# Kernel tuning notes

Measured on AMD Instinct MI355X. Metric: run time of the kernel, lower is better.

Reference implementation:

```python
import jax, jax.numpy as jnp
import numpy as np

# Config: 4 sparse batch items, each with 2048 active voxels (uniform-length case
# of sparse full self-attention). channels=1024, heads=16, head_dim=64.
B_SEQ, L, H, D = 4, 2048, 16, 64
C = H * D  # 1024
N = B_SEQ * L  # 8192
EPS = 1e-12  # F.normalize eps


def setup_inputs() -> dict:
    key = jax.random.key(0)
    ks = jax.random.split(key, 6)
    s = 1.0 / np.sqrt(C)
    return {
        "x": jax.random.normal(ks[0], (N, C), dtype=jnp.float32),
        "W_qkv": jax.random.normal(ks[1], (C, 3 * C), dtype=jnp.float32) * s,
        "b_qkv": jnp.zeros((3 * C,), dtype=jnp.float32),
        "gamma_q": jnp.ones((H, D), dtype=jnp.float32),
        "gamma_k": jnp.ones((H, D), dtype=jnp.float32),
        "W_out": jax.random.normal(ks[2], (C, C), dtype=jnp.float32) * s,
        "b_out": jnp.zeros((C,), dtype=jnp.float32),
    }


def _qk_rms_norm(t, gamma):
    # SparseMultiHeadRMSNorm: L2-normalize last dim, scale by gamma[h,d] * sqrt(D)
    norm = jnp.maximum(jnp.linalg.norm(t, axis=-1, keepdims=True), EPS)
    return (t / norm) * gamma * (D ** 0.5)


def reference(x, W_qkv, b_qkv, gamma_q, gamma_k, W_out, b_out):
    qkv = x @ W_qkv + b_qkv                       # [N, 3C]
    qkv = qkv.reshape(B_SEQ, L, 3, H, D)          # fused pre-reshape
    q, k, v = qkv[:, :, 0], qkv[:, :, 1], qkv[:, :, 2]  # [B,L,H,D]
    q = _qk_rms_norm(q, gamma_q)
    k = _qk_rms_norm(k, gamma_k)
    # full scaled dot-product attention within each sparse batch item
    scores = jnp.einsum('blhd,bmhd->bhlm', q, k) / (D ** 0.5)
    attn = jax.nn.softmax(scores, axis=-1)
    h = jnp.einsum('bhlm,bmhd->blhd', attn, v)    # [B,L,H,D]
    h = h.reshape(N, C)
    return h @ W_out + b_out
```

## Files before the change

### kernel.cpp

```cpp
#include <hip/hip_runtime.h>

using u16 = unsigned short;

typedef float  f32x4  __attribute__((ext_vector_type(4)));
typedef float  f32x16 __attribute__((ext_vector_type(16)));
typedef __bf16 bf16x8 __attribute__((ext_vector_type(8)));
typedef short  s16x8  __attribute__((ext_vector_type(8)));

#define DEVI __device__ __forceinline__

constexpr int TOK = 8192;
constexpr int CIN = 1024;
constexpr int C3  = 3072;
constexpr int NH  = 16;
constexpr int HD  = 64;
constexpr int SL  = 2048;
constexpr int BH  = 64;

constexpr float LOG2E = 1.4426950408889634f;

DEVI u16 f2bf(float x) {
  unsigned u = __builtin_bit_cast(unsigned, x);
  u += 0x7FFFu + ((u >> 16) & 1u);
  return (u16)(u >> 16);
}

DEVI f32x4 mfma16(s16x8 a, s16x8 b, f32x4 c) {
  return __builtin_amdgcn_mfma_f32_16x16x32_bf16(
      __builtin_bit_cast(bf16x8, a), __builtin_bit_cast(bf16x8, b), c, 0, 0, 0);
}

DEVI f32x16 mfma32(s16x8 a, s16x8 b, f32x16 c) {
  return __builtin_amdgcn_mfma_f32_32x32x16_bf16(
      __builtin_bit_cast(bf16x8, a), __builtin_bit_cast(bf16x8, b), c, 0, 0, 0);
}

DEVI void gload_lds16(const void* g, void* l) {
  __builtin_amdgcn_global_load_lds(
      (const __attribute__((address_space(1))) unsigned int*)g,
      (__attribute__((address_space(3))) unsigned int*)l, 16, 0, 0);
}

DEVI unsigned cvtpk(float lo, float hi) {
  unsigned r;
  asm("v_cvt_pk_bf16_f32 %0, %1, %2" : "=v"(r) : "v"(lo), "v"(hi));
  return r;
}

DEVI void plswap(unsigned& a, unsigned& b) {
  asm("v_permlane32_swap_b32 %0, %1" : "+v"(a), "+v"(b));
}

__global__ __launch_bounds__(256) void k_cvt_x(const float* __restrict__ x,
                                               u16* __restrict__ xb) {
  const int total = TOK * CIN / 4;
  for (int i = blockIdx.x * 256 + threadIdx.x; i < total; i += gridDim.x * 256) {
    float4 v = ((const float4*)x)[i];
    ushort4 o;
    o.x = f2bf(v.x); o.y = f2bf(v.y); o.z = f2bf(v.z); o.w = f2bf(v.w);
    ((ushort4*)xb)[i] = o;
  }
}

__global__ __launch_bounds__(256) void k_transpose(const float* __restrict__ in,
                                                   u16* __restrict__ out,
                                                   int R, int C) {
  __shared__ u16 t[64][72];
  int rt = R >> 6;
  int tr = (blockIdx.x % rt) << 6;
  int tc = (blockIdx.x / rt) << 6;
  int tid = threadIdx.x;
#pragma unroll
  for (int k2 = 0; k2 < 16; k2++) {
    int idx = k2 * 256 + tid;
    int r = idx >> 6, c = idx & 63;
    t[r][c] = f2bf(in[(size_t)(tr + r) * C + tc + c]);
  }
  __syncthreads();
#pragma unroll
  for (int k2 = 0; k2 < 16; k2++) {
    int idx = k2 * 256 + tid;
    int r = idx >> 6, c = idx & 63;
    out[(size_t)(tc + r) * R + tr + c] = t[c][r];
  }
}

__global__ __launch_bounds__(256) void k_gemm_qkv(
    const u16* __restrict__ A, const u16* __restrict__ Bt,
    const float* __restrict__ bias, const float* __restrict__ gq,
    const float* __restrict__ gk,
    u16* __restrict__ Qn, u16* __restrict__ Kn, u16* __restrict__ Vt) {
  constexpr int BK = 32, K = 1024, NT = C3 / 128;
  __shared__ u16 As[128 * BK], Bs[128 * BK];
  const int bm = (blockIdx.x / NT) * 128, bn = (blockIdx.x % NT) * 128;
  const int tid = threadIdx.x, lane = tid & 63, w = tid >> 6;
  const int l15 = lane & 15, g = lane >> 4;
  const int wr = (w >> 1) * 64, wc = (w & 1) * 64;

  f32x4 acc[4][4];
#pragma unroll
  for (int i = 0; i < 4; i++)
#pragma unroll
    for (int j = 0; j < 4; j++) acc[i][j] = f32x4{0.f, 0.f, 0.f, 0.f};

  const int srow = tid >> 2, scol = (tid & 3) * 8;
  const u16* Ag = A + (size_t)(bm + srow) * K + scol;
  const u16* Bg = Bt + (size_t)(bn + srow) * K + scol;
  char* AsB = (char*)As;
  char* BsB = (char*)Bs;

  for (int k0 = 0; k0 < K; k0 += BK) {
    __syncthreads();
    gload_lds16(Ag + k0,          AsB + w * 1024);
    gload_lds16(Ag + 64 * K + k0, AsB + 4096 + w * 1024);
    gload_lds16(Bg + k0,          BsB + w * 1024);
    gload_lds16(Bg + 64 * K + k0, BsB + 4096 + w * 1024);
    __syncthreads();
    s16x8 af[4], bf[4];
#pragma unroll
    for (int mf = 0; mf < 4; mf++)
      af[mf] = *(const s16x8*)(As + (wr + mf * 16 + l15) * BK + g * 8);
#pragma unroll
    for (int nf = 0; nf < 4; nf++)
      bf[nf] = *(const s16x8*)(Bs + (wc + nf * 16 + l15) * BK + g * 8);
#pragma unroll
    for (int mf = 0; mf < 4; mf++)
#pragma unroll
      for (int nf = 0; nf < 4; nf++)
        acc[mf][nf] = mfma16(af[mf], bf[nf], acc[mf][nf]);
  }

  const int c0 = bn + wc;
  const int sec = c0 >> 10;
  const int head = (c0 & 1023) >> 6;
  float bv[4], gv[4];
#pragma unroll
  for (int nf = 0; nf < 4; nf++) {
    bv[nf] = bias[c0 + nf * 16 + l15];
    gv[nf] = 1.f;
    if (sec == 0) gv[nf] = gq[head * 64 + nf * 16 + l15];
    if (sec == 1) gv[nf] = gk[head * 64 + nf * 16 + l15];
  }
#pragma unroll
  for (int mf = 0; mf < 4; mf++) {
#pragma unroll
    for (int nf = 0; nf < 4; nf++)
#pragma unroll
      for (int r = 0; r < 4; r++) acc[mf][nf][r] += bv[nf];
    if (sec < 2) {
#pragma unroll
      for (int r = 0; r < 4; r++) {
        float ss = 0.f;
#pragma unroll
        for (int nf = 0; nf < 4; nf++) ss += acc[mf][nf][r] * acc[mf][nf][r];
        ss += __shfl_xor(ss, 1); ss += __shfl_xor(ss, 2);
        ss += __shfl_xor(ss, 4); ss += __shfl_xor(ss, 8);
        float nrm = fmaxf(sqrtf(ss), 1e-12f);
        float f = (sec == 0 ? LOG2E : 8.0f) / nrm;
#pragma unroll
        for (int nf = 0; nf < 4; nf++) acc[mf][nf][r] *= f;
      }
    }
    int rbase = bm + wr + mf * 16 + 4 * g;
#pragma unroll
    for (int r = 0; r < 4; r++) {
      int row = rbase + r;
      int b = row >> 11, tok = row & 2047;
      int bh = b * NH + head;
#pragma unroll
      for (int nf = 0; nf < 4; nf++) {
        int d = nf * 16 + l15;
        u16 val = f2bf(acc[mf][nf][r] * gv[nf]);
        if (sec == 0)      Qn[((size_t)bh * SL + tok) * HD + d] = val;
        else if (sec == 1) Kn[((size_t)bh * SL + tok) * HD + d] = val;
        else               Vt[((size_t)bh * HD + d) * SL + tok] = val;
      }
    }
  }
}

__global__ __launch_bounds__(512) void k_attn(const u16* __restrict__ Qn,
                                              const u16* __restrict__ Kn,
                                              const u16* __restrict__ Vt,
                                              u16* __restrict__ hm) {
  __shared__ __align__(16) char KL[2][8192];
  __shared__ __align__(16) char VL[2][8192];
  const int bh = blockIdx.x & 63, qb = blockIdx.x >> 6;
  const int tid = threadIdx.x, w = tid >> 6, lane = tid & 63;
  const int l31 = lane & 31, h = lane >> 5;
  const int qr0 = qb * 256 + w * 32;

  const int sr  = tid >> 3;
  const int scb = ((tid & 7) << 4) ^ ((sr & 7) << 4);
  const char* kst = (const char*)(Kn + (size_t)bh * SL * HD) + (size_t)sr * 128 + scb;
  const char* vst = (const char*)(Vt + (size_t)bh * HD * SL) + (size_t)sr * 4096 + scb;
  char* kl0 = KL[0] + (w << 10);
  char* vl0 = VL[0] + (w << 10);
  char* kl1 = KL[1] + (w << 10);
  char* vl1 = VL[1] + (w << 10);

  const u16* Qb = Qn + ((size_t)bh * SL + qr0 + l31) * HD + 8 * h;
  s16x8 qf[4];
#pragma unroll
  for (int ks = 0; ks < 4; ks++) qf[ks] = *(const s16x8*)(Qb + ks * 16);

  const int lb = l31 * 128 + ((h << 4) ^ ((l31 & 7) << 4));

  f32x16 o0, o1;
#pragma unroll
  for (int i = 0; i < 16; i++) { o0[i] = 0.f; o1[i] = 0.f; }
  float mr = -1e30f, lr = 0.f;

  gload_lds16(kst, kl0);
  gload_lds16(vst, vl0);
  __syncthreads();

  for (int it = 0; it < 32; ++it) {
    const char* KB = (it & 1) ? KL[1] : KL[0];
    const char* VB = (it & 1) ? VL[1] : VL[0];
    if (it < 31) {
      const size_t ko = (size_t)(it + 1) << 13;
      const size_t vo = (size_t)(it + 1) << 7;
      gload_lds16(kst + ko, (it & 1) ? kl0 : kl1);
      gload_lds16(vst + vo, (it & 1) ? vl0 : vl1);
    }

    f32x16 s0, s1;
#pragma unroll
    for (int i = 0; i < 16; i++) { s0[i] = 0.f; s1[i] = 0.f; }
    __builtin_amdgcn_s_setprio(1);
#pragma unroll
    for (int ks = 0; ks < 4; ks++) {
      const s16x8 ka  = *(const s16x8*)(KB + (lb ^ (ks << 5)));
      const s16x8 kb2 = *(const s16x8*)(KB + 4096 + (lb ^ (ks << 5)));
      s0 = mfma32(ka, qf[ks], s0);
      s1 = mfma32(kb2, qf[ks], s1);
    }
    __builtin_amdgcn_s_setprio(0);

    float mx8[8];
#pragma unroll
    for (int i = 0; i < 8; i++)
      mx8[i] = fmaxf(fmaxf(s0[i], s0[i + 8]), fmaxf(s1[i], s1[i + 8]));
    float m0 = fmaxf(fmaxf(mx8[0], mx8[1]), fmaxf(mx8[2], mx8[3]));
    float m1 = fmaxf(fmaxf(mx8[4], mx8[5]), fmaxf(mx8[6], mx8[7]));
    float bm = fmaxf(m0, m1);
    bm = fmaxf(bm, __shfl_xor(bm, 32));

    if (!__all(bm <= mr + 8.f)) {
      const float mn = fmaxf(mr, bm);
      const float sc = __builtin_amdgcn_exp2f(mr - mn);
      mr = mn;
      lr *= sc;
#pragma unroll
      for (int i = 0; i < 16; i++) { o0[i] *= sc; o1[i] *= sc; }
    }
#pragma unroll
    for (int i = 0; i < 16; i++) s0[i] = __builtin_amdgcn_exp2f(s0[i] - mr);
#pragma unroll
    for (int i = 0; i < 16; i++) s1[i] = __builtin_amdgcn_exp2f(s1[i] - mr);
    float sm8[8];
#pragma unroll
    for (int i = 0; i < 8; i++)
      sm8[i] = (s0[i] + s0[i + 8]) + (s1[i] + s1[i + 8]);
    lr += ((sm8[0] + sm8[1]) + (sm8[2] + sm8[3])) +
          ((sm8[4] + sm8[5]) + (sm8[6] + sm8[7]));

    union PBu { unsigned u[4]; s16x8 v; } pb;
#define MK_PB(SV, B)                              \
    {                                             \
      unsigned a0 = cvtpk(SV[B + 0], SV[B + 1]);  \
      unsigned c0 = cvtpk(SV[B + 4], SV[B + 5]);  \
      plswap(a0, c0);                             \
      unsigned a1 = cvtpk(SV[B + 2], SV[B + 3]);  \
      unsigned c1 = cvtpk(SV[B + 6], SV[B + 7]);  \
      plswap(a1, c1);                             \
      pb.u[0] = a0; pb.u[1] = a1; pb.u[2] = c0; pb.u[3] = c1; \
    }
#define PV_STEP(KS)                                            \
    {                                                          \
      const s16x8 va = *(const s16x8*)(VB + (lb ^ (KS << 5))); \
      const s16x8 vb = *(const s16x8*)(VB + 4096 + (lb ^ (KS << 5))); \
      __builtin_amdgcn_s_setprio(1);                           \
      o0 = mfma32(va, pb.v, o0);                               \
      o1 = mfma32(vb, pb.v, o1);                               \
      __builtin_amdgcn_s_setprio(0);                           \
    }
    MK_PB(s0, 0) PV_STEP(0)
    MK_PB(s0, 8) PV_STEP(1)
    MK_PB(s1, 0) PV_STEP(2)
    MK_PB(s1, 8) PV_STEP(3)
#undef MK_PB
#undef PV_STEP

    __syncthreads();
  }

  const float ltot = lr + __shfl_xor(lr, 32);
  const float inv = 1.f / ltot;
  const int bq = bh >> 4, hh = bh & 15;
  u16* hb = hm + ((size_t)bq * SL + qr0 + l31) * CIN + hh * HD;
#pragma unroll
  for (int rg = 0; rg < 4; rg++) {
    const int d0 = 8 * rg + 4 * h;
    unsigned lo = cvtpk(o0[4 * rg + 0] * inv, o0[4 * rg + 1] * inv);
    unsigned hi = cvtpk(o0[4 * rg + 2] * inv, o0[4 * rg + 3] * inv);
    *(unsigned long long*)(hb + d0) =
        (unsigned long long)lo | ((unsigned long long)hi << 32);
    unsigned lo1 = cvtpk(o1[4 * rg + 0] * inv, o1[4 * rg + 1] * inv);
    unsigned hi1 = cvtpk(o1[4 * rg + 2] * inv, o1[4 * rg + 3] * inv);
    *(unsigned long long*)(hb + 32 + d0) =
        (unsigned long long)lo1 | ((unsigned long long)hi1 << 32);
  }
}

__global__ __launch_bounds__(256) void k_gemm_out(
    const u16* __restrict__ A, const u16* __restrict__ Bt,
    const float* __restrict__ bias, float* __restrict__ out) {
  constexpr int BK = 32, K = 1024, NT = CIN / 128;
  __shared__ u16 As[128 * BK], Bs[128 * BK];
  const int bm = (blockIdx.x / NT) * 128, bn = (blockIdx.x % NT) * 128;
  const int tid = threadIdx.x, lane = tid & 63, w = tid >> 6;
  const int l15 = lane & 15, g = lane >> 4;
  const int wr = (w >> 1) * 64, wc = (w & 1) * 64;

  f32x4 acc[4][4];
#pragma unroll
  for (int i = 0; i < 4; i++)
#pragma unroll
    for (int j = 0; j < 4; j++) acc[i][j] = f32x4{0.f, 0.f, 0.f, 0.f};

  const int srow = tid >> 2, scol = (tid & 3) * 8;
  const u16* Ag = A + (size_t)(bm + srow) * K + scol;
  const u16* Bg = Bt + (size_t)(bn + srow) * K + scol;
  char* AsB = (char*)As;
  char* BsB = (char*)Bs;

  for (int k0 = 0; k0 < K; k0 += BK) {
    __syncthreads();
    gload_lds16(Ag + k0,          AsB + w * 1024);
    gload_lds16(Ag + 64 * K + k0, AsB + 4096 + w * 1024);
    gload_lds16(Bg + k0,          BsB + w * 1024);
    gload_lds16(Bg + 64 * K + k0, BsB + 4096 + w * 1024);
    __syncthreads();
    s16x8 af[4], bf[4];
#pragma unroll
    for (int mf = 0; mf < 4; mf++)
      af[mf] = *(const s16x8*)(As + (wr + mf * 16 + l15) * BK + g * 8);
#pragma unroll
    for (int nf = 0; nf < 4; nf++)
      bf[nf] = *(const s16x8*)(Bs + (wc + nf * 16 + l15) * BK + g * 8);
#pragma unroll
    for (int mf = 0; mf < 4; mf++)
#pragma unroll
      for (int nf = 0; nf < 4; nf++)
        acc[mf][nf] = mfma16(af[mf], bf[nf], acc[mf][nf]);
  }

  float bv[4];
#pragma unroll
  for (int nf = 0; nf < 4; nf++) bv[nf] = bias[bn + wc + nf * 16 + l15];
#pragma unroll
  for (int mf = 0; mf < 4; mf++)
#pragma unroll
    for (int r = 0; r < 4; r++) {
      int row = bm + wr + mf * 16 + 4 * g + r;
#pragma unroll
      for (int nf = 0; nf < 4; nf++)
        out[(size_t)row * CIN + bn + wc + nf * 16 + l15] = acc[mf][nf][r] + bv[nf];
    }
}

extern "C" void kernel_launch(void* const* d_in, const int* in_sizes, int n_in,
                              void* d_out, int out_size, void* d_ws, size_t ws_size,
                              hipStream_t stream) {
  const float* x    = (const float*)d_in[0];
  const float* Wqkv = (const float*)d_in[1];
  const float* bqkv = (const float*)d_in[2];
  const float* gq   = (const float*)d_in[3];
  const float* gk   = (const float*)d_in[4];
  const float* Wout = (const float*)d_in[5];
  const float* bout = (const float*)d_in[6];
  float* out = (float*)d_out;

  char* ws = (char*)d_ws;
  u16* xb  = (u16*)(ws);
  u16* wqT = (u16*)(ws + 16777216);
  u16* woT = (u16*)(ws + 23068672);
  u16* Qn  = (u16*)(ws + 25165824);
  u16* Kn  = (u16*)(ws + 41943040);
  u16* Vt  = (u16*)(ws + 58720256);
  u16* hm  = (u16*)(ws + 75497472);

  k_cvt_x<<<2048, 256, 0, stream>>>(x, xb);
  k_transpose<<<(1024 / 64) * (3072 / 64), 256, 0, stream>>>(Wqkv, wqT, 1024, 3072);
  k_transpose<<<(1024 / 64) * (1024 / 64), 256, 0, stream>>>(Wout, woT, 1024, 1024);
  k_gemm_qkv<<<(TOK / 128) * (C3 / 128), 256, 0, stream>>>(xb, wqT, bqkv, gq, gk, Qn, Kn, Vt);
  k_attn<<<BH * (SL / 256), 512, 0, stream>>>(Qn, Kn, Vt, hm);
  k_gemm_out<<<(TOK / 128) * (CIN / 128), 256, 0, stream>>>(hm, woT, bout, out);
}
```

Baseline: 228.5 us.

## Double-buffer LDS tiles in QKV and output GEMMs to overlap loads with MFMA

Both projection GEMMs now keep two LDS buffers and issue the global-to-LDS loads for the next K-slice before the MFMAs on the current slice. This removes one barrier per iteration and hides global load latency behind compute. The MFMA block is also wrapped in s_setprio to raise wave priority during matrix math. LDS use per block doubles, which may reduce occupancy. Correctness depends on the async LDS loads completing before the single barrier at the end of each iteration.

```diff
diff --git a/kernel.cpp b/kernel.cpp
--- a/kernel.cpp
+++ b/kernel.cpp
@@ -90,8 +90,8 @@
     const float* __restrict__ bias, const float* __restrict__ gq,
     const float* __restrict__ gk,
     u16* __restrict__ Qn, u16* __restrict__ Kn, u16* __restrict__ Vt) {
-  constexpr int BK = 32, K = 1024, NT = C3 / 128;
-  __shared__ u16 As[128 * BK], Bs[128 * BK];
+  constexpr int BK = 32, K = 1024, NT = C3 / 128, NIT = K / BK;
+  __shared__ u16 As[2][128 * BK], Bs[2][128 * BK];
   const int bm = (blockIdx.x / NT) * 128, bn = (blockIdx.x % NT) * 128;
   const int tid = threadIdx.x, lane = tid & 63, w = tid >> 6;
   const int l15 = lane & 15, g = lane >> 4;
@@ -106,29 +106,40 @@
   const int srow = tid >> 2, scol = (tid & 3) * 8;
   const u16* Ag = A + (size_t)(bm + srow) * K + scol;
   const u16* Bg = Bt + (size_t)(bn + srow) * K + scol;
-  char* AsB = (char*)As;
-  char* BsB = (char*)Bs;
-
-  for (int k0 = 0; k0 < K; k0 += BK) {
+
+#define STAGE_G1(BUF, K0)                                            \
+  {                                                                  \
+    char* AsB = (char*)As[BUF];                                      \
+    char* BsB = (char*)Bs[BUF];                                      \
+    gload_lds16(Ag + (K0),          AsB + w * 1024);                 \
+    gload_lds16(Ag + 64 * K + (K0), AsB + 4096 + w * 1024);          \
+    gload_lds16(Bg + (K0),          BsB + w * 1024);                 \
+    gload_lds16(Bg + 64 * K + (K0), BsB + 4096 + w * 1024);          \
+  }
+
+  STAGE_G1(0, 0)
+  __syncthreads();
+
+  for (int t = 0; t < NIT; ++t) {
+    const int cur = t & 1;
+    if (t < NIT - 1) STAGE_G1(cur ^ 1, (t + 1) * BK)
+    s16x8 af[4], bfx[4];
+#pragma unroll
+    for (int mf = 0; mf < 4; mf++)
+      af[mf] = *(const s16x8*)(As[cur] + (wr + mf * 16 + l15) * BK + g * 8);
+#pragma unroll
+    for (int nf = 0; nf < 4; nf++)
+      bfx[nf] = *(const s16x8*)(Bs[cur] + (wc + nf * 16 + l15) * BK + g * 8);
+    __builtin_amdgcn_s_setprio(1);
+#pragma unroll
+    for (int mf = 0; mf < 4; mf++)
+#pragma unroll
+      for (int nf = 0; nf < 4; nf++)
+        acc[mf][nf] = mfma16(af[mf], bfx[nf], acc[mf][nf]);
+    __builtin_amdgcn_s_setprio(0);
     __syncthreads();
-    gload_lds16(Ag + k0,          AsB + w * 1024);
-    gload_lds16(Ag + 64 * K + k0, AsB + 4096 + w * 1024);
-    gload_lds16(Bg + k0,          BsB + w * 1024);
-    gload_lds16(Bg + 64 * K + k0, BsB + 4096 + w * 1024);
-    __syncthreads();
-    s16x8 af[4], bf[4];
-#pragma unroll
-    for (int mf = 0; mf < 4; mf++)
-      af[mf] = *(const s16x8*)(As + (wr + mf * 16 + l15) * BK + g * 8);
-#pragma unroll
-    for (int nf = 0; nf < 4; nf++)
-      bf[nf] = *(const s16x8*)(Bs + (wc + nf * 16 + l15) * BK + g * 8);
-#pragma unroll
-    for (int mf = 0; mf < 4; mf++)
-#pragma unroll
-      for (int nf = 0; nf < 4; nf++)
-        acc[mf][nf] = mfma16(af[mf], bf[nf], acc[mf][nf]);
-  }
+  }
+#undef STAGE_G1
 
   const int c0 = bn + wc;
   const int sec = c0 >> 10;
@@ -317,8 +328,8 @@
 __global__ __launch_bounds__(256) void k_gemm_out(
     const u16* __restrict__ A, const u16* __restrict__ Bt,
     const float* __restrict__ bias, float* __restrict__ out) {
-  constexpr int BK = 32, K = 1024, NT = CIN / 128;
-  __shared__ u16 As[128 * BK], Bs[128 * BK];
+  constexpr int BK = 32, K = 1024, NT = CIN / 128, NIT = K / BK;
+  __shared__ u16 As[2][128 * BK], Bs[2][128 * BK];
   const int bm = (blockIdx.x / NT) * 128, bn = (blockIdx.x % NT) * 128;
   const int tid = threadIdx.x, lane = tid & 63, w = tid >> 6;
   const int l15 = lane & 15, g = lane >> 4;
@@ -333,29 +344,40 @@
   const int srow = tid >> 2, scol = (tid & 3) * 8;
   const u16* Ag = A + (size_t)(bm + srow) * K + scol;
   const u16* Bg = Bt + (size_t)(bn + srow) * K + scol;
-  char* AsB = (char*)As;
-  char* BsB = (char*)Bs;
-
-  for (int k0 = 0; k0 < K; k0 += BK) {
+
+#define STAGE_G2(BUF, K0)                                            \
+  {                                                                  \
+    char* AsB = (char*)As[BUF];                                      \
+    char* BsB = (char*)Bs[BUF];                                      \
+    gload_lds16(Ag + (K0),          AsB + w * 1024);                 \
+    gload_lds16(Ag + 64 * K + (K0), AsB + 4096 + w * 1024);          \
+    gload_lds16(Bg + (K0),          BsB + w * 1024);                 \
+    gload_lds16(Bg + 64 * K + (K0), BsB + 4096 + w * 1024);          \
+  }
+
+  STAGE_G2(0, 0)
+  __syncthreads();
+
+  for (int t = 0; t < NIT; ++t) {
+    const int cur = t & 1;
+    if (t < NIT - 1) STAGE_G2(cur ^ 1, (t + 1) * BK)
+    s16x8 af[4], bfx[4];
+#pragma unroll
+    for (int mf = 0; mf < 4; mf++)
+      af[mf] = *(const s16x8*)(As[cur] + (wr + mf * 16 + l15) * BK + g * 8);
+#pragma unroll
+    for (int nf = 0; nf < 4; nf++)
+      bfx[nf] = *(const s16x8*)(Bs[cur] + (wc + nf * 16 + l15) * BK + g * 8);
+    __builtin_amdgcn_s_setprio(1);
+#pragma unroll
+    for (int mf = 0; mf < 4; mf++)
+#pragma unroll
+      for (int nf = 0; nf < 4; nf++)
+        acc[mf][nf] = mfma16(af[mf], bfx[nf], acc[mf][nf]);
+    __builtin_amdgcn_s_setprio(0);
     __syncthreads();
-    gload_lds16(Ag + k0,          AsB + w * 1024);
-    gload_lds16(Ag + 64 * K + k0, AsB + 4096 + w * 1024);
-    gload_lds16(Bg + k0,          BsB + w * 1024);
-    gload_lds16(Bg + 64 * K + k0, BsB + 4096 + w * 1024);
-    __syncthreads();
-    s16x8 af[4], bf[4];
-#pragma unroll
-    for (int mf = 0; mf < 4; mf++)
-      af[mf] = *(const s16x8*)(As + (wr + mf * 16 + l15) * BK + g * 8);
-#pragma unroll
-    for (int nf = 0; nf < 4; nf++)
-      bf[nf] = *(const s16x8*)(Bs + (wc + nf * 16 + l15) * BK + g * 8);
-#pragma unroll
-    for (int mf = 0; mf < 4; mf++)
-#pragma unroll
-      for (int nf = 0; nf < 4; nf++)
-        acc[mf][nf] = mfma16(af[mf], bf[nf], acc[mf][nf]);
-  }
+  }
+#undef STAGE_G2
 
   float bv[4];
 #pragma unroll
```

After: 244.2 us. 1.07x slower.

## Rewrite QKV and output GEMMs with 256x128 tiles and triple-buffered LDS pipeline

Applied to the files above, without the earlier changes.

Both projection GEMMs now use 512-thread blocks with 256x128 output tiles and a K step of 64. Global-to-LDS copies are triple-buffered with explicit vmcnt waits so loads overlap MFMA work, and the LDS layout is XOR-swizzled to avoid bank conflicts. Block indices are remapped so neighbouring blocks share input tiles in L2, and wave priority is raised around the MFMA bursts. In exchange, each block uses about 147KB of LDS, which limits occupancy to a single block per CU.

```diff
diff --git a/kernel.cpp b/kernel.cpp
--- a/kernel.cpp
+++ b/kernel.cpp
@@ -85,17 +85,77 @@
   }
 }
 
-__global__ __launch_bounds__(256) void k_gemm_qkv(
+#define STAGE6(BUF, KT)                                                  \
+  { char* Ld = L + (BUF) * 49152;                                        \
+    const size_t ko = (size_t)(KT) * 128;                                \
+    gload_lds16(Ab + ko,          Ld + wb);                              \
+    gload_lds16(Ab + ko + 131072, Ld + 8192 + wb);                       \
+    gload_lds16(Ab + ko + 262144, Ld + 16384 + wb);                      \
+    gload_lds16(Ab + ko + 393216, Ld + 24576 + wb);                      \
+    gload_lds16(Bb + ko,          Ld + 32768 + wb);                      \
+    gload_lds16(Bb + ko + 131072, Ld + 40960 + wb); }
+
+#define KBODY(KT, DOSTAGE, VMSTR)                                        \
+  {                                                                      \
+    if (DOSTAGE) STAGE6(((KT) + 2) % 3, (KT) + 2)                        \
+    asm volatile("s_waitcnt " VMSTR ::: "memory");                       \
+    __builtin_amdgcn_s_barrier();                                        \
+    const char* Lb = L + ((KT) % 3) * 49152;                             \
+    s16x8 af[4][2], bfr[4][2];                                           \
+    _Pragma("unroll")                                                    \
+    for (int mf = 0; mf < 4; mf++) {                                     \
+      af[mf][0] = *(const s16x8*)(Lb + aoff + mf * 2048 + cx0);          \
+      af[mf][1] = *(const s16x8*)(Lb + aoff + mf * 2048 + (cx0 ^ 64));   \
+    }                                                                    \
+    _Pragma("unroll")                                                    \
+    for (int nf = 0; nf < 4; nf++) {                                     \
+      bfr[nf][0] = *(const s16x8*)(Lb + boff + nf * 2048 + cx0);         \
+      bfr[nf][1] = *(const s16x8*)(Lb + boff + nf * 2048 + (cx0 ^ 64));  \
+    }                                                                    \
+    __builtin_amdgcn_s_setprio(1);                                       \
+    _Pragma("unroll")                                                    \
+    for (int ks = 0; ks < 2; ks++)                                       \
+      _Pragma("unroll")                                                  \
+      for (int mf = 0; mf < 4; mf++)                                     \
+        _Pragma("unroll")                                                \
+        for (int nf = 0; nf < 4; nf++)                                   \
+          acc[mf][nf] = mfma16(af[mf][ks], bfr[nf][ks], acc[mf][nf]);    \
+    __builtin_amdgcn_s_setprio(0);                                       \
+    __builtin_amdgcn_s_barrier();                                        \
+  }
+
+DEVI void gemm_mainloop(const char* Ab, const char* Bb, char* L,
+                        int wb, int aoff, int boff, int cx0,
+                        f32x4 (&acc)[4][4]) {
+  STAGE6(0, 0)
+  STAGE6(1, 1)
+#pragma unroll
+  for (int kt = 0; kt < 14; ++kt) KBODY(kt, 1, "vmcnt(12)")
+  KBODY(14, 0, "vmcnt(6)")
+  KBODY(15, 0, "vmcnt(0)")
+}
+
+__global__ __launch_bounds__(512, 2) void k_gemm_qkv(
     const u16* __restrict__ A, const u16* __restrict__ Bt,
     const float* __restrict__ bias, const float* __restrict__ gq,
     const float* __restrict__ gk,
     u16* __restrict__ Qn, u16* __restrict__ Kn, u16* __restrict__ Vt) {
-  constexpr int BK = 32, K = 1024, NT = C3 / 128;
-  __shared__ u16 As[128 * BK], Bs[128 * BK];
-  const int bm = (blockIdx.x / NT) * 128, bn = (blockIdx.x % NT) * 128;
+  __shared__ __align__(16) char Lsh[3][49152];
+  int bid = blockIdx.x;
+  bid = (bid & 7) * 96 + (bid >> 3);
+  const int bm = (bid / 24) * 256, bn = (bid % 24) * 128;
   const int tid = threadIdx.x, lane = tid & 63, w = tid >> 6;
   const int l15 = lane & 15, g = lane >> 4;
-  const int wr = (w >> 1) * 64, wc = (w & 1) * 64;
+  const int wr4 = w >> 1, wc2 = w & 1;
+
+  const int rA  = tid >> 3;
+  const int scb = ((tid & 7) << 4) ^ ((rA & 7) << 4);
+  const char* Ab = (const char*)A + (size_t)(bm + rA) * 2048 + scb;
+  const char* Bb = (const char*)Bt + (size_t)(bn + rA) * 2048 + scb;
+  const int wb   = w << 10;
+  const int aoff = (wr4 * 64 + l15) * 128;
+  const int boff = 32768 + (wc2 * 64 + l15) * 128;
+  const int cx0  = (g ^ (l15 & 7)) << 4;
 
   f32x4 acc[4][4];
 #pragma unroll
@@ -103,34 +163,9 @@
 #pragma unroll
     for (int j = 0; j < 4; j++) acc[i][j] = f32x4{0.f, 0.f, 0.f, 0.f};
 
-  const int srow = tid >> 2, scol = (tid & 3) * 8;
-  const u16* Ag = A + (size_t)(bm + srow) * K + scol;
-  const u16* Bg = Bt + (size_t)(bn + srow) * K + scol;
-  char* AsB = (char*)As;
-  char* BsB = (char*)Bs;
-
-  for (int k0 = 0; k0 < K; k0 += BK) {
-    __syncthreads();
-    gload_lds16(Ag + k0,          AsB + w * 1024);
-    gload_lds16(Ag + 64 * K + k0, AsB + 4096 + w * 1024);
-    gload_lds16(Bg + k0,          BsB + w * 1024);
-    gload_lds16(Bg + 64 * K + k0, BsB + 4096 + w * 1024);
-    __syncthreads();
-    s16x8 af[4], bf[4];
-#pragma unroll
-    for (int mf = 0; mf < 4; mf++)
-      af[mf] = *(const s16x8*)(As + (wr + mf * 16 + l15) * BK + g * 8);
-#pragma unroll
-    for (int nf = 0; nf < 4; nf++)
-      bf[nf] = *(const s16x8*)(Bs + (wc + nf * 16 + l15) * BK + g * 8);
-#pragma unroll
-    for (int mf = 0; mf < 4; mf++)
-#pragma unroll
-      for (int nf = 0; nf < 4; nf++)
-        acc[mf][nf] = mfma16(af[mf], bf[nf], acc[mf][nf]);
-  }
-
-  const int c0 = bn + wc;
+  gemm_mainloop(Ab, Bb, (char*)Lsh, wb, aoff, boff, cx0, acc);
+
+  const int c0 = bn + wc2 * 64;
   const int sec = c0 >> 10;
   const int head = (c0 & 1023) >> 6;
   float bv[4], gv[4];
@@ -161,7 +196,7 @@
         for (int nf = 0; nf < 4; nf++) acc[mf][nf][r] *= f;
       }
     }
-    int rbase = bm + wr + mf * 16 + 4 * g;
+    int rbase = bm + wr4 * 64 + mf * 16 + 4 * g;
 #pragma unroll
     for (int r = 0; r < 4; r++) {
       int row = rbase + r;
@@ -177,6 +212,49 @@
       }
     }
   }
+}
+
+__global__ __launch_bounds__(512, 2) void k_gemm_out(
+    const u16* __restrict__ A, const u16* __restrict__ Bt,
+    const float* __restrict__ bias, float* __restrict__ out) {
+  __shared__ __align__(16) char Lsh[3][49152];
+  int bid = blockIdx.x;
+  bid = (bid & 7) * 32 + (bid >> 3);
+  const int bm = (bid / 8) * 256, bn = (bid % 8) * 128;
+  const int tid = threadIdx.x, lane = tid & 63, w = tid >> 6;
+  const int l15 = lane & 15, g = lane >> 4;
+  const int wr4 = w >> 1, wc2 = w & 1;
+
+  const int rA  = tid >> 3;
+  const int scb = ((tid & 7) << 4) ^ ((rA & 7) << 4);
+  const char* Ab = (const char*)A + (size_t)(bm + rA) * 2048 + scb;
+  const char* Bb = (const char*)Bt + (size_t)(bn + rA) * 2048 + scb;
+  const int wb   = w << 10;
+  const int aoff = (wr4 * 64 + l15) * 128;
+  const int boff = 32768 + (wc2 * 64 + l15) * 128;
+  const int cx0  = (g ^ (l15 & 7)) << 4;
+
+  f32x4 acc[4][4];
+#pragma unroll
+  for (int i = 0; i < 4; i++)
+#pragma unroll
+    for (int j = 0; j < 4; j++) acc[i][j] = f32x4{0.f, 0.f, 0.f, 0.f};
+
+  gemm_mainloop(Ab, Bb, (char*)Lsh, wb, aoff, boff, cx0, acc);
+
+  float bv[4];
+#pragma unroll
+  for (int nf = 0; nf < 4; nf++) bv[nf] = bias[bn + wc2 * 64 + nf * 16 + l15];
+#pragma unroll
+  for (int mf = 0; mf < 4; mf++)
+#pragma unroll
+    for (int r = 0; r < 4; r++) {
+      int row = bm + wr4 * 64 + mf * 16 + 4 * g + r;
+#pragma unroll
+      for (int nf = 0; nf < 4; nf++)
+        out[(size_t)row * CIN + bn + wc2 * 64 + nf * 16 + l15] =
+            acc[mf][nf][r] + bv[nf];
+    }
 }
 
 __global__ __launch_bounds__(512) void k_attn(const u16* __restrict__ Qn,
@@ -312,63 +390,6 @@
     *(unsigned long long*)(hb + 32 + d0) =
         (unsigned long long)lo1 | ((unsigned long long)hi1 << 32);
   }
-}
-
-__global__ __launch_bounds__(256) void k_gemm_out(
-    const u16* __restrict__ A, const u16* __restrict__ Bt,
-    const float* __restrict__ bias, float* __restrict__ out) {
-  constexpr int BK = 32, K = 1024, NT = CIN / 128;
-  __shared__ u16 As[128 * BK], Bs[128 * BK];
-  const int bm = (blockIdx.x / NT) * 128, bn = (blockIdx.x % NT) * 128;
-  const int tid = threadIdx.x, lane = tid & 63, w = tid >> 6;
-  const int l15 = lane & 15, g = lane >> 4;
-  const int wr = (w >> 1) * 64, wc = (w & 1) * 64;
-
-  f32x4 acc[4][4];
-#pragma unroll
-  for (int i = 0; i < 4; i++)
-#pragma unroll
-    for (int j = 0; j < 4; j++) acc[i][j] = f32x4{0.f, 0.f, 0.f, 0.f};
-
-  const int srow = tid >> 2, scol = (tid & 3) * 8;
-  const u16* Ag = A + (size_t)(bm + srow) * K + scol;
-  const u16* Bg = Bt + (size_t)(bn + srow) * K + scol;
-  char* AsB = (char*)As;
-  char* BsB = (char*)Bs;
-
-  for (int k0 = 0; k0 < K; k0 += BK) {
-    __syncthreads();
-    gload_lds16(Ag + k0,          AsB + w * 1024);
-    gload_lds16(Ag + 64 * K + k0, AsB + 4096 + w * 1024);
-    gload_lds16(Bg + k0,          BsB + w * 1024);
-    gload_lds16(Bg + 64 * K + k0, BsB + 4096 + w * 1024);
-    __syncthreads();
-    s16x8 af[4], bf[4];
-#pragma unroll
-    for (int mf = 0; mf < 4; mf++)
-      af[mf] = *(const s16x8*)(As + (wr + mf * 16 + l15) * BK + g * 8);
-#pragma unroll
-    for (int nf = 0; nf < 4; nf++)
-      bf[nf] = *(const s16x8*)(Bs + (wc + nf * 16 + l15) * BK + g * 8);
-#pragma unroll
-    for (int mf = 0; mf < 4; mf++)
-#pragma unroll
-      for (int nf = 0; nf < 4; nf++)
-        acc[mf][nf] = mfma16(af[mf], bf[nf], acc[mf][nf]);
-  }
-
-  float bv[4];
-#pragma unroll
-  for (int nf = 0; nf < 4; nf++) bv[nf] = bias[bn + wc + nf * 16 + l15];
-#pragma unroll
-  for (int mf = 0; mf < 4; mf++)
-#pragma unroll
-    for (int r = 0; r < 4; r++) {
-      int row = bm + wr + mf * 16 + 4 * g + r;
-#pragma unroll
-      for (int nf = 0; nf < 4; nf++)
-        out[(size_t)row * CIN + bn + wc + nf * 16 + l15] = acc[mf][nf][r] + bv[nf];
-    }
 }
 
 extern "C" void kernel_launch(void* const* d_in, const int* in_sizes, int n_in,
@@ -395,7 +416,7 @@
   k_cvt_x<<<2048, 256, 0, stream>>>(x, xb);
   k_transpose<<<(1024 / 64) * (3072 / 64), 256, 0, stream>>>(Wqkv, wqT, 1024, 3072);
   k_transpose<<<(1024 / 64) * (1024 / 64), 256, 0, stream>>>(Wout, woT, 1024, 1024);
-  k_gemm_qkv<<<(TOK / 128) * (C3 / 128), 256, 0, stream>>>(xb, wqT, bqkv, gq, gk, Qn, Kn, Vt);
+  k_gemm_qkv<<<(TOK / 256) * (C3 / 128), 512, 0, stream>>>(xb, wqT, bqkv, gq, gk, Qn, Kn, Vt);
   k_attn<<<BH * (SL / 256), 512, 0, stream>>>(Qn, Kn, Vt, hm);
-  k_gemm_out<<<(TOK / 128) * (CIN / 128), 256, 0, stream>>>(hm, woT, bout, out);
-}
+  k_gemm_out<<<(TOK / 256) * (CIN / 128), 512, 0, stream>>>(hm, woT, bout, out);
+}
```

After: 209.9 us. -8.2%, faster.
